# Optimization experiments

Measured on AMD Instinct MI355X. Metric: run time of the kernel, lower is better.

The kernel has to match this reference:

```python
import jax, jax.numpy as jnp
import numpy as np

H = 512; W = 512; WL = 8; SS = 4; DIM = 128; HEADS = 4; HD = DIM // HEADS; HID = 512
N = WL * WL                      # tokens per window = 64
NW = (H // WL) * (W // WL)       # num windows = 4096
EPS = 1e-5


def _rel_pos_index():
    # standard Swin relative position index for a WLxWL window
    coords = np.stack(np.meshgrid(np.arange(WL), np.arange(WL), indexing='ij')).reshape(2, -1)  # [2, N]
    rel = (coords[:, :, None] - coords[:, None, :]).transpose(1, 2, 0)  # [N, N, 2]
    rel[..., 0] += WL - 1
    rel[..., 1] += WL - 1
    rel[..., 0] *= 2 * WL - 1
    return jnp.asarray(rel.sum(-1))  # [N, N] in [0, (2WL-1)^2)


def _shift_attn_mask():
    # region ids 0/1/2 along each axis per the h_slices/w_slices loop, cnt = 3*h_id + w_id
    ids = np.zeros(H)
    ids[H - WL:H - SS] = 1
    ids[H - SS:] = 2
    img = 3.0 * ids[:, None] + ids[None, :]                     # [H, W]
    wnd = img.reshape(H // WL, WL, W // WL, WL).transpose(0, 2, 1, 3).reshape(NW, N)
    diff = wnd[:, None, :] - wnd[:, :, None]                    # [NW, N, N]
    return jnp.asarray(np.where(diff != 0, -100.0, 0.0).astype(np.float32))


REL_IDX = _rel_pos_index()
ATTN_MASK = _shift_attn_mask()


def _layernorm(v, w, b):
    mu = v.mean(-1, keepdims=True)
    var = v.var(-1, keepdims=True)
    return (v - mu) * jax.lax.rsqrt(var + EPS) * w + b


def setup_inputs() -> dict:
    key = jax.random.key(0)
    ks = jax.random.split(key, 10)
    s = 0.02
    return {
        'x': jax.random.normal(ks[0], (H * W, DIM), dtype=jnp.float32),
        'ln1_w': jnp.ones((DIM,), jnp.float32), 'ln1_b': jnp.zeros((DIM,), jnp.float32),
        'qkv_w': jax.random.normal(ks[1], (3 * DIM, DIM), jnp.float32) * s,
        'qkv_b': jnp.zeros((3 * DIM,), jnp.float32),
        'rel_bias': jax.random.normal(ks[2], ((2 * WL - 1) ** 2, HEADS), jnp.float32) * s,
        'proj_w': jax.random.normal(ks[3], (DIM, DIM), jnp.float32) * s,
        'proj_b': jnp.zeros((DIM,), jnp.float32),
        'ln2_w': jnp.ones((DIM,), jnp.float32), 'ln2_b': jnp.zeros((DIM,), jnp.float32),
        'mlp_w1': jax.random.normal(ks[4], (HID, DIM), jnp.float32) * s,
        'mlp_b1': jnp.zeros((HID,), jnp.float32),
        'mlp_w2': jax.random.normal(ks[5], (DIM, HID), jnp.float32) * s,
        'mlp_b2': jnp.zeros((DIM,), jnp.float32),
    }


def reference(x, ln1_w, ln1_b, qkv_w, qkv_b, rel_bias, proj_w, proj_b,
              ln2_w, ln2_b, mlp_w1, mlp_b1, mlp_w2, mlp_b2):
    skip = x
    xn = _layernorm(x, ln1_w, ln1_b).reshape(H, W, DIM)
    # cyclic shift
    xs = jnp.roll(xn, shift=(-SS, -SS), axis=(0, 1))
    # window partition -> [NW, N, DIM]
    xw = xs.reshape(H // WL, WL, W // WL, WL, DIM).transpose(0, 2, 1, 3, 4).reshape(NW, N, DIM)
    # qkv projection, split heads
    qkv = (xw @ qkv_w.T + qkv_b).reshape(NW, N, 3, HEADS, HD)
    q, k, v = qkv[:, :, 0], qkv[:, :, 1], qkv[:, :, 2]   # each [NW, N, HEADS, HD]
    scale = HD ** -0.5
    scores = jnp.einsum('wnhd,wmhd->whnm', q, k) * scale   # [NW, HEADS, N, N]
    bias = rel_bias[REL_IDX].transpose(2, 0, 1)            # [HEADS, N, N]
    scores = scores + bias[None] + ATTN_MASK[:, None]
    attn = jax.nn.softmax(scores, axis=-1)
    out = jnp.einsum('whnm,wmhd->wnhd', attn, v).reshape(NW, N, DIM)
    out = out @ proj_w.T + proj_b
    # window reverse
    xr = out.reshape(H // WL, W // WL, WL, WL, DIM).transpose(0, 2, 1, 3, 4).reshape(H, W, DIM)
    # reverse cyclic shift
    xr = jnp.roll(xr, shift=(SS, SS), axis=(0, 1)).reshape(H * W, DIM)
    x1 = skip + xr
    # FFN block
    h = _layernorm(x1, ln2_w, ln2_b)
    h = jax.nn.gelu(h @ mlp_w1.T + mlp_b1) @ mlp_w2.T + mlp_b2
    return x1 + h
```

## Files before the change

### kernel.cpp

```cpp
#include <hip/hip_runtime.h>
#include <hip/hip_bf16.h>


typedef __bf16 bf16x8 __attribute__((ext_vector_type(8)));
typedef __bf16 bf16x2 __attribute__((ext_vector_type(2)));
typedef float f32x4 __attribute__((ext_vector_type(4)));

#define MFMA16(a, b, c) __builtin_amdgcn_mfma_f32_16x16x32_bf16(a, b, c, 0, 0, 0)
#define LGKM_BARRIER() do { \
    asm volatile("s_waitcnt lgkmcnt(0)" ::: "memory"); \
    __builtin_amdgcn_s_barrier(); } while (0)

#define SS 4
#define XS 136
#define QKS 40
#define PSS 72
#define X1S 140

#define QKV_W_OFF 0
#define PROJ_W_OFF 98304
#define W1_OFF 131072
#define W2_OFF 262144
#define BIAS_OFF 393216

__device__ __forceinline__ int regid(int u) { return (u >= 508) ? 2 : ((u >= 504) ? 1 : 0); }

__global__ __launch_bounds__(256) void prep_kernel(
    const float* __restrict__ qkv_w, const float* __restrict__ proj_w,
    const float* __restrict__ w1, const float* __restrict__ w2,
    const float* __restrict__ rel_bias, unsigned char* __restrict__ ws) {
  int tid = blockIdx.x * 256 + threadIdx.x;
  __bf16* qw = (__bf16*)(ws + QKV_W_OFF);
  __bf16* pw = (__bf16*)(ws + PROJ_W_OFF);
  __bf16* w1b = (__bf16*)(ws + W1_OFF);
  __bf16* w2b = (__bf16*)(ws + W2_OFF);
  float* btbl = (float*)(ws + BIAS_OFF);
  if (tid < 49152) {
    int e = tid & 7, lane = (tid >> 3) & 63, kk = (tid >> 9) & 3;
    int f = tid >> 11;
    int h = f / 6, nt = f % 6;
    int j = (nt >> 1) * 128 + h * 32 + (nt & 1) * 16 + (lane & 15);
    int k = kk * 32 + (lane >> 4) * 8 + e;
    qw[tid] = (__bf16)qkv_w[j * 128 + k];
  }
  if (tid < 16384) {
    int e = tid & 7, lane = (tid >> 3) & 63, kk = (tid >> 9) & 3;
    int nt2 = (tid >> 11) & 1, wid = (tid >> 12) & 3;
    int j = wid * 32 + nt2 * 16 + (lane & 15);
    int k = kk * 32 + (lane >> 4) * 8 + e;
    pw[tid] = (__bf16)proj_w[j * 128 + k];
  }
  if (tid < 65536) {
    {
      int e = tid & 7, lane = (tid >> 3) & 63, kk = (tid >> 9) & 3;
      int nt = (tid >> 11) & 1, wid = (tid >> 12) & 7, c = (tid >> 15) & 1;
      int j = c * 256 + wid * 32 + nt * 16 + (lane & 15);
      int k = kk * 32 + (lane >> 4) * 8 + e;
      w1b[tid] = (__bf16)w1[j * 128 + k]; }
    { int e = tid & 7, lane = (tid >> 3) & 63, kk = (tid >> 9) & 15, wid = (tid >> 13) & 7;
      int j = wid * 16 + (lane & 15);
      int k = kk * 32 + (lane >> 4) * 8 + e;
      w2b[tid] = (__bf16)w2[j * 512 + k]; }
  }
  if (tid < 16384) {
    int i = tid & 3, lane = (tid >> 2) & 63;
    int kt = (tid >> 8) & 3, qt = (tid >> 10) & 3, h = (tid >> 12) & 3;
    int n = qt * 16 + (lane & 15);
    int m = kt * 16 + (lane >> 4) * 4 + i;
    int idx = ((n >> 3) - (m >> 3) + 7) * 15 + ((n & 7) - (m & 7) + 7);
    btbl[tid] = rel_bias[idx * 4 + h];
  }
}

__global__ __launch_bounds__(256, 2) void attn_kernel(
    const float* __restrict__ x, const float* __restrict__ ln1_w, const float* __restrict__ ln1_b,
    const float* __restrict__ qkv_b, const float* __restrict__ proj_b,
    const unsigned char* __restrict__ ws, float* __restrict__ out) {
  __shared__ __attribute__((aligned(16))) __bf16 xn[64 * XS];
  __shared__ __attribute__((aligned(16))) __bf16 wreg[4][5120];
  __shared__ __attribute__((aligned(16))) __bf16 vt[4][32 * PSS];
  __shared__ __attribute__((aligned(16))) int rid[64];

  const int w = blockIdx.x;
  const int wi = w >> 6, wj = w & 63;
  const int tid = threadIdx.x;
  const int wid = tid >> 6, lane = tid & 63;
  const int lr = lane & 15, lk = lane >> 4;
  const bool edge = (wi == 63) || (wj == 63);
  const f32x4 zero4 = {0.f, 0.f, 0.f, 0.f};

  const __bf16* qw = (const __bf16*)(ws + QKV_W_OFF);
  bf16x8 bw[6][4];
  float qb[6];
#pragma unroll
  for (int nt = 0; nt < 6; nt++) {
    qb[nt] = qkv_b[(nt >> 1) * 128 + wid * 32 + (nt & 1) * 16 + lr];
#pragma unroll
    for (int kk = 0; kk < 4; kk++)
      bw[nt][kk] = *(const bf16x8*)(qw + ((wid * 6 + nt) * 4 + kk) * 512 + lane * 8);
  }

  {
    int n = tid >> 2, q = tid & 3;
    int r = n >> 3, c = n & 7;
    int io = (wi * 8 + r + SS) & 511;
    int jo = (wj * 8 + c + SS) & 511;
    size_t gid = (size_t)io * 512 + jo;
    const float4* xp = (const float4*)(x + gid * 128 + q * 32);
    float4 xv[8];
    float s = 0.f, s2 = 0.f;
#pragma unroll
    for (int t = 0; t < 8; t++) {
      float4 v = xp[t]; xv[t] = v;
      s += v.x + v.y + v.z + v.w;
      s2 += v.x * v.x + v.y * v.y + v.z * v.z + v.w * v.w;
    }
    s += __shfl_xor(s, 1); s += __shfl_xor(s, 2);
    s2 += __shfl_xor(s2, 1); s2 += __shfl_xor(s2, 2);
    float mean = s * (1.f / 128.f);
    float var = s2 * (1.f / 128.f) - mean * mean;
    float rstd = rsqrtf(var + 1e-5f);
    const float4* wv = (const float4*)(ln1_w + q * 32);
    const float4* bv = (const float4*)(ln1_b + q * 32);
    __bf16* dst = xn + n * XS + q * 32;
#pragma unroll
    for (int t = 0; t < 8; t++) {
      float4 wt = wv[t], bt = bv[t], v = xv[t];
      dst[t * 4 + 0] = (__bf16)((v.x - mean) * rstd * wt.x + bt.x);
      dst[t * 4 + 1] = (__bf16)((v.y - mean) * rstd * wt.y + bt.y);
      dst[t * 4 + 2] = (__bf16)((v.z - mean) * rstd * wt.z + bt.z);
      dst[t * 4 + 3] = (__bf16)((v.w - mean) * rstd * wt.w + bt.w);
    }
    if (q == 0) rid[n] = 3 * regid(wi * 8 + r) + regid(wj * 8 + c);
  }
  LGKM_BARRIER();

  {
    const float scale = 0.17677669529663687f;
    __bf16* qbase = &wreg[wid][0];
    __bf16* kbase = &wreg[wid][2560];
    __bf16* vbase = &vt[wid][0];
#pragma unroll
    for (int st = 0; st < 4; st++) {
      bf16x8 a[4];
#pragma unroll
      for (int kk = 0; kk < 4; kk++)
        a[kk] = *(const bf16x8*)(xn + (st * 16 + lr) * XS + kk * 32 + lk * 8);
#pragma unroll
      for (int nt = 0; nt < 6; nt++) {
        f32x4 acc = zero4;
#pragma unroll
        for (int kk = 0; kk < 4; kk++) acc = MFMA16(a[kk], bw[nt][kk], acc);
        float bias = qb[nt];
        int dl = (nt & 1) * 16 + lr;
        if (nt < 2) {
#pragma unroll
          for (int i = 0; i < 4; i++)
            qbase[(st * 16 + lk * 4 + i) * QKS + dl] = (__bf16)((acc[i] + bias) * scale);
        } else if (nt < 4) {
#pragma unroll
          for (int i = 0; i < 4; i++)
            kbase[(st * 16 + lk * 4 + i) * QKS + dl] = (__bf16)(acc[i] + bias);
        } else {
#pragma unroll
          for (int i = 0; i < 4; i++)
            vbase[dl * PSS + st * 16 + lk * 4 + i] = (__bf16)(acc[i] + bias);
        }
      }
    }
  }

  const __bf16* pw = (const __bf16*)(ws + PROJ_W_OFF);
  bf16x8 pwf[2][4];
  float pb2[2];
#pragma unroll
  for (int nt2 = 0; nt2 < 2; nt2++) {
    pb2[nt2] = proj_b[wid * 32 + nt2 * 16 + lr];
#pragma unroll
    for (int kk = 0; kk < 4; kk++)
      pwf[nt2][kk] = *(const bf16x8*)(pw + ((wid * 2 + nt2) * 4 + kk) * 512 + lane * 8);
  }
  const float* btbl = (const float*)(ws + BIAS_OFF);
  f32x4 bc[4][4];
#pragma unroll
  for (int qt = 0; qt < 4; qt++)
#pragma unroll
    for (int kt = 0; kt < 4; kt++)
      bc[qt][kt] = *(const f32x4*)(btbl + ((wid * 4 + qt) * 4 + kt) * 256 + lane * 4);

  int gidx[4][4];
#pragma unroll
  for (int st = 0; st < 4; st++)
#pragma unroll
    for (int i = 0; i < 4; i++) {
      int rr = st * 16 + lk * 4 + i;
      int io = (wi * 8 + (rr >> 3) + SS) & 511;
      int jo = (wj * 8 + (rr & 7) + SS) & 511;
      gidx[st][i] = io * 512 + jo;
    }
  float xres[4][2][4];
#pragma unroll
  for (int st = 0; st < 4; st++)
#pragma unroll
    for (int nt2 = 0; nt2 < 2; nt2++)
#pragma unroll
      for (int i = 0; i < 4; i++)
        xres[st][nt2][i] = x[(size_t)gidx[st][i] * 128 + wid * 32 + nt2 * 16 + lr];

  {
    __bf16* reg0 = &wreg[wid][0];
    bf16x8 kf[4], qf[4], vf[2][2];
#pragma unroll
    for (int kt = 0; kt < 4; kt++)
      kf[kt] = *(const bf16x8*)(reg0 + 2560 + (kt * 16 + lr) * QKS + lk * 8);
#pragma unroll
    for (int qt = 0; qt < 4; qt++)
      qf[qt] = *(const bf16x8*)(reg0 + (qt * 16 + lr) * QKS + lk * 8);
#pragma unroll
    for (int dt = 0; dt < 2; dt++)
#pragma unroll
      for (int kk = 0; kk < 2; kk++)
        vf[dt][kk] = *(const bf16x8*)(&vt[wid][(dt * 16 + lr) * PSS + kk * 32 + lk * 8]);
    asm volatile("s_waitcnt lgkmcnt(0)" ::: "memory");
    __builtin_amdgcn_sched_barrier(0);

    int4 rk[4];
    if (edge) {
#pragma unroll
      for (int kt = 0; kt < 4; kt++) rk[kt] = *(const int4*)&rid[kt * 16 + lk * 4];
    }

#pragma unroll
    for (int qt = 0; qt < 4; qt++) {
      f32x4 s[4];
#pragma unroll
      for (int kt = 0; kt < 4; kt++) s[kt] = MFMA16(kf[kt], qf[qt], bc[qt][kt]);
      if (edge) {
        int rq = rid[qt * 16 + lr];
#pragma unroll
        for (int kt = 0; kt < 4; kt++) {
          s[kt][0] += (rk[kt].x != rq) ? -100.f : 0.f;
          s[kt][1] += (rk[kt].y != rq) ? -100.f : 0.f;
          s[kt][2] += (rk[kt].z != rq) ? -100.f : 0.f;
          s[kt][3] += (rk[kt].w != rq) ? -100.f : 0.f;
        }
      }
      float ex[4][4];
      float sum = 0.f;
#pragma unroll
      for (int kt = 0; kt < 4; kt++) {
#pragma unroll
        for (int i = 0; i < 4; i++) { ex[kt][i] = __expf(s[kt][i]); sum += ex[kt][i]; }
      }
      sum += __shfl_xor(sum, 16);
      sum += __shfl_xor(sum, 32);
      float inv = __builtin_amdgcn_rcpf(sum);
      __bf16* psrow = reg0 + (qt * 16 + lr) * PSS;
#pragma unroll
      for (int kt = 0; kt < 4; kt++) {
        bf16x2 p01 = {(__bf16)(ex[kt][0] * inv), (__bf16)(ex[kt][1] * inv)};
        bf16x2 p23 = {(__bf16)(ex[kt][2] * inv), (__bf16)(ex[kt][3] * inv)};
        *(bf16x2*)(psrow + kt * 16 + lk * 4) = p01;
        *(bf16x2*)(psrow + kt * 16 + lk * 4 + 2) = p23;
      }
#pragma unroll
      for (int dt = 0; dt < 2; dt++) {
        bf16x8 pa0 = *(const bf16x8*)(reg0 + (qt * 16 + lr) * PSS + lk * 8);
        bf16x8 pa1 = *(const bf16x8*)(reg0 + (qt * 16 + lr) * PSS + 32 + lk * 8);
        f32x4 acc = MFMA16(pa0, vf[dt][0], zero4);
        acc = MFMA16(pa1, vf[dt][1], acc);
#pragma unroll
        for (int i = 0; i < 4; i++)
          reg0[qt * 1152 + (lk * 4 + i) * QKS + dt * 16 + lr] = (__bf16)acc[i];
      }
    }
  }
  LGKM_BARRIER();

  {
#pragma unroll
    for (int st = 0; st < 4; st++) {
      bf16x8 ao[4];
#pragma unroll
      for (int kk = 0; kk < 4; kk++)
        ao[kk] = *(const bf16x8*)(&wreg[kk][st * 1152 + lr * QKS + lk * 8]);
#pragma unroll
      for (int nt2 = 0; nt2 < 2; nt2++) {
        f32x4 acc = zero4;
#pragma unroll
        for (int kk = 0; kk < 4; kk++) acc = MFMA16(ao[kk], pwf[nt2][kk], acc);
        int j = wid * 32 + nt2 * 16 + lr;
#pragma unroll
        for (int i = 0; i < 4; i++) {
          size_t off = (size_t)gidx[st][i] * 128 + j;
          out[off] = xres[st][nt2][i] + acc[i] + pb2[nt2];
        }
      }
    }
  }
}

__device__ __forceinline__ float gelu_sig(float x) {
  float e = exp2f(x * -2.4554826f);
  return x * __builtin_amdgcn_rcpf(1.f + e);
}

__global__ __launch_bounds__(512, 4) void mlp_kernel(
    const float* __restrict__ ln2_w, const float* __restrict__ ln2_b,
    const float* __restrict__ mlp_b1, const float* __restrict__ mlp_b2,
    const unsigned char* __restrict__ ws, float* __restrict__ out) {
  __shared__ __attribute__((aligned(16))) __bf16 xn[64 * 128];
  __shared__ __attribute__((aligned(16))) __bf16 hb[64 * 256];
  __shared__ __attribute__((aligned(16))) __bf16 x1b[64 * X1S];
  const int tid = threadIdx.x;
  const int wid = tid >> 6, lane = tid & 63;
  const int lr = lane & 15, lk = lane >> 4;
  const f32x4 zero4 = {0.f, 0.f, 0.f, 0.f};
  const int row0 = blockIdx.x * 64;

  const __bf16* w1r = (const __bf16*)(ws + W1_OFF);
  const __bf16* w2r = (const __bf16*)(ws + W2_OFF);

  float b1v[2][2];
#pragma unroll
  for (int c = 0; c < 2; c++)
#pragma unroll
    for (int nt = 0; nt < 2; nt++)
      b1v[c][nt] = mlp_b1[c * 256 + wid * 32 + nt * 16 + lr];
  float b2v = mlp_b2[wid * 16 + lr];

  {
    int n = tid >> 3, q = tid & 7;
    const float4* xp = (const float4*)(out + (size_t)(row0 + n) * 128 + q * 16);
    float4 xv[4];
    float s = 0.f, s2 = 0.f;
#pragma unroll
    for (int t = 0; t < 4; t++) {
      float4 v = xp[t]; xv[t] = v;
      s += v.x + v.y + v.z + v.w;
      s2 += v.x * v.x + v.y * v.y + v.z * v.z + v.w * v.w;
    }
    s += __shfl_xor(s, 1); s += __shfl_xor(s, 2); s += __shfl_xor(s, 4);
    s2 += __shfl_xor(s2, 1); s2 += __shfl_xor(s2, 2); s2 += __shfl_xor(s2, 4);
    float mean = s * (1.f / 128.f);
    float var = s2 * (1.f / 128.f) - mean * mean;
    float rstd = rsqrtf(var + 1e-5f);
    const float4* wv = (const float4*)(ln2_w + q * 16);
    const float4* bv = (const float4*)(ln2_b + q * 16);
    bf16x8 o[2], r[2];
#pragma unroll
    for (int t = 0; t < 4; t++) {
      float4 wt = wv[t], bt = bv[t], v = xv[t];
      o[t >> 1][(t & 1) * 4 + 0] = (__bf16)((v.x - mean) * rstd * wt.x + bt.x);
      o[t >> 1][(t & 1) * 4 + 1] = (__bf16)((v.y - mean) * rstd * wt.y + bt.y);
      o[t >> 1][(t & 1) * 4 + 2] = (__bf16)((v.z - mean) * rstd * wt.z + bt.z);
      o[t >> 1][(t & 1) * 4 + 3] = (__bf16)((v.w - mean) * rstd * wt.w + bt.w);
      r[t >> 1][(t & 1) * 4 + 0] = (__bf16)v.x;
      r[t >> 1][(t & 1) * 4 + 1] = (__bf16)v.y;
      r[t >> 1][(t & 1) * 4 + 2] = (__bf16)v.z;
      r[t >> 1][(t & 1) * 4 + 3] = (__bf16)v.w;
    }
    *(bf16x8*)(xn + n * 128 + (((q * 2 + 0) ^ (n & 15)) << 3)) = o[0];
    *(bf16x8*)(xn + n * 128 + (((q * 2 + 1) ^ (n & 15)) << 3)) = o[1];
    *(bf16x8*)(x1b + n * X1S + q * 16) = r[0];
    *(bf16x8*)(x1b + n * X1S + q * 16 + 8) = r[1];
  }
  __syncthreads();

  f32x4 macc[4] = {zero4, zero4, zero4, zero4};

#pragma unroll 1
  for (int c = 0; c < 2; c++) {
    {
      bf16x8 w1f[2][4];
#pragma unroll
      for (int nt = 0; nt < 2; nt++)
#pragma unroll
        for (int kk = 0; kk < 4; kk++)
          w1f[nt][kk] = *(const bf16x8*)(w1r + (((c * 8 + wid) * 2 + nt) * 4 + kk) * 512 + lane * 8);
#pragma unroll
      for (int st = 0; st < 4; st++) {
        bf16x8 a1[4];
#pragma unroll
        for (int kk = 0; kk < 4; kk++)
          a1[kk] = *(const bf16x8*)(xn + (st * 16 + lr) * 128 + (((kk * 4 + lk) ^ lr) << 3));
#pragma unroll
        for (int nt = 0; nt < 2; nt++) {
          f32x4 acc = zero4;
#pragma unroll
          for (int kk = 0; kk < 4; kk++) acc = MFMA16(a1[kk], w1f[nt][kk], acc);
          int slot = wid * 4 + nt * 2 + (lr >> 3);
#pragma unroll
          for (int i = 0; i < 4; i++) {
            int row = st * 16 + lk * 4 + i;
            hb[row * 256 + ((slot ^ (row & 15)) << 3) + (lr & 7)] =
                (__bf16)gelu_sig(acc[i] + b1v[c][nt]);
          }
        }
      }
    }
    __syncthreads();

    {
      bf16x8 w2f[8];
#pragma unroll
      for (int kks = 0; kks < 8; kks++)
        w2f[kks] = *(const bf16x8*)(w2r + (wid * 16 + c * 8 + kks) * 512 + lane * 8);
#pragma unroll
      for (int st = 0; st < 4; st++) {
#pragma unroll
        for (int kks = 0; kks < 8; kks++) {
          bf16x8 ah = *(const bf16x8*)(hb + (st * 16 + lr) * 256 + (((kks * 4 + lk) ^ lr) << 3));
          macc[st] = MFMA16(ah, w2f[kks], macc[st]);
        }
      }
    }
    __syncthreads();
  }

  {
    float* stg = (float*)hb;
#pragma unroll
    for (int st = 0; st < 4; st++)
#pragma unroll
      for (int i = 0; i < 4; i++) {
        int row = st * 16 + lk * 4 + i;
        int col = wid * 16 + lr;
        int sp = (col >> 2) ^ (((row >> 2) & 7) << 2);
        float x1v = (float)x1b[row * X1S + col];
        stg[row * 128 + sp * 4 + (col & 3)] = x1v + macc[st][i] + b2v;
      }
    __syncthreads();
    int half = lane >> 5, sl = lane & 31;
#pragma unroll
    for (int it = 0; it < 4; it++) {
      int row = wid * 8 + it * 2 + half;
      int sp = sl ^ (((row >> 2) & 7) << 2);
      f32x4 v = *(const f32x4*)(stg + row * 128 + sp * 4);
      *(f32x4*)(out + (size_t)(row0 + row) * 128 + sl * 4) = v;
    }
  }
}

extern "C" void kernel_launch(void* const* d_in, const int* in_sizes, int n_in,
                              void* d_out, int out_size, void* d_ws, size_t ws_size,
                              hipStream_t stream) {
  const float* x      = (const float*)d_in[0];
  const float* ln1_w  = (const float*)d_in[1];
  const float* ln1_b  = (const float*)d_in[2];
  const float* qkv_w  = (const float*)d_in[3];
  const float* qkv_b  = (const float*)d_in[4];
  const float* rel_b  = (const float*)d_in[5];
  const float* proj_w = (const float*)d_in[6];
  const float* proj_b = (const float*)d_in[7];
  const float* ln2_w  = (const float*)d_in[8];
  const float* ln2_b  = (const float*)d_in[9];
  const float* mlp_w1 = (const float*)d_in[10];
  const float* mlp_b1 = (const float*)d_in[11];
  const float* mlp_w2 = (const float*)d_in[12];
  const float* mlp_b2 = (const float*)d_in[13];
  float* out = (float*)d_out;
  unsigned char* ws = (unsigned char*)d_ws;

  prep_kernel<<<256, 256, 0, stream>>>(qkv_w, proj_w, mlp_w1, mlp_w2, rel_b, ws);
  attn_kernel<<<4096, 256, 0, stream>>>(x, ln1_w, ln1_b, qkv_b, proj_b, ws, out);
  mlp_kernel<<<4096, 512, 0, stream>>>(ln2_w, ln2_b, mlp_b1, mlp_b2, ws, out);
}
```

Baseline: 256.3 us.

## Split MLP hidden dimension into four chunks to shrink LDS and raise occupancy

The MLP kernel now processes the 512-wide hidden layer in four 128-wide chunks instead of two 256-wide ones, halving the hidden staging buffer in shared memory. It also reorders the W1 weight layout to match, folds the biases into the accumulator initial values, packs the shared buffers into one array, and raises the launch-bounds occupancy hint from 4 to 6. The aim is more resident workgroups per CU to hide memory latency, at the cost of twice as many barrier-separated phases per block.

New measurement: 238.8 us. 1.07x faster.

```diff
diff --git a/kernel.cpp b/kernel.cpp
--- a/kernel.cpp
+++ b/kernel.cpp
@@ -15,7 +15,7 @@
 #define XS 136
 #define QKS 40
 #define PSS 72
-#define X1S 140
+#define X1S 136
 
 #define QKV_W_OFF 0
 #define PROJ_W_OFF 98304
@@ -53,11 +53,12 @@
   if (tid < 65536) {
     {
       int e = tid & 7, lane = (tid >> 3) & 63, kk = (tid >> 9) & 3;
-      int nt = (tid >> 11) & 1, wid = (tid >> 12) & 7, c = (tid >> 15) & 1;
-      int j = c * 256 + wid * 32 + nt * 16 + (lane & 15);
+      int g = (tid >> 11) & 31;
+      int j = g * 16 + (lane & 15);
       int k = kk * 32 + (lane >> 4) * 8 + e;
       w1b[tid] = (__bf16)w1[j * 128 + k]; }
-    { int e = tid & 7, lane = (tid >> 3) & 63, kk = (tid >> 9) & 15, wid = (tid >> 13) & 7;
+    {
+      int e = tid & 7, lane = (tid >> 3) & 63, kk = (tid >> 9) & 15, wid = (tid >> 13) & 7;
       int j = wid * 16 + (lane & 15);
       int k = kk * 32 + (lane >> 4) * 8 + e;
       w2b[tid] = (__bf16)w2[j * 512 + k]; }
@@ -305,29 +306,27 @@
   return x * __builtin_amdgcn_rcpf(1.f + e);
 }
 
-__global__ __launch_bounds__(512, 4) void mlp_kernel(
+__global__ __launch_bounds__(512, 6) void mlp_kernel(
     const float* __restrict__ ln2_w, const float* __restrict__ ln2_b,
     const float* __restrict__ mlp_b1, const float* __restrict__ mlp_b2,
     const unsigned char* __restrict__ ws, float* __restrict__ out) {
-  __shared__ __attribute__((aligned(16))) __bf16 xn[64 * 128];
-  __shared__ __attribute__((aligned(16))) __bf16 hb[64 * 256];
-  __shared__ __attribute__((aligned(16))) __bf16 x1b[64 * X1S];
+  __shared__ __attribute__((aligned(16))) unsigned char smem[50176];
+  __bf16* xn  = (__bf16*)smem;
+  __bf16* hb  = (__bf16*)(smem + 16384);
+  __bf16* x1b = (__bf16*)(smem + 32768);
   const int tid = threadIdx.x;
   const int wid = tid >> 6, lane = tid & 63;
   const int lr = lane & 15, lk = lane >> 4;
-  const f32x4 zero4 = {0.f, 0.f, 0.f, 0.f};
   const int row0 = blockIdx.x * 64;
+  const int col = wid * 16 + lr;
 
   const __bf16* w1r = (const __bf16*)(ws + W1_OFF);
   const __bf16* w2r = (const __bf16*)(ws + W2_OFF);
 
-  float b1v[2][2];
-#pragma unroll
-  for (int c = 0; c < 2; c++)
-#pragma unroll
-    for (int nt = 0; nt < 2; nt++)
-      b1v[c][nt] = mlp_b1[c * 256 + wid * 32 + nt * 16 + lr];
-  float b2v = mlp_b2[wid * 16 + lr];
+  float b1v[4];
+#pragma unroll
+  for (int c = 0; c < 4; c++) b1v[c] = mlp_b1[c * 128 + wid * 16 + lr];
+  float b2v = mlp_b2[col];
 
   {
     int n = tid >> 3, q = tid & 7;
@@ -367,50 +366,48 @@
   }
   __syncthreads();
 
-  f32x4 macc[4] = {zero4, zero4, zero4, zero4};
+  f32x4 macc[4];
+#pragma unroll
+  for (int st = 0; st < 4; st++) macc[st] = (f32x4){b2v, b2v, b2v, b2v};
 
 #pragma unroll 1
-  for (int c = 0; c < 2; c++) {
+  for (int c = 0; c < 4; c++) {
     {
-      bf16x8 w1f[2][4];
-#pragma unroll
-      for (int nt = 0; nt < 2; nt++)
-#pragma unroll
-        for (int kk = 0; kk < 4; kk++)
-          w1f[nt][kk] = *(const bf16x8*)(w1r + (((c * 8 + wid) * 2 + nt) * 4 + kk) * 512 + lane * 8);
+      bf16x8 w1f[4];
+#pragma unroll
+      for (int kk = 0; kk < 4; kk++)
+        w1f[kk] = *(const bf16x8*)(w1r + ((c * 8 + wid) * 4 + kk) * 512 + lane * 8);
+      f32x4 bini = {b1v[c], b1v[c], b1v[c], b1v[c]};
+      int slot = wid * 2 + (lr >> 3);
 #pragma unroll
       for (int st = 0; st < 4; st++) {
         bf16x8 a1[4];
 #pragma unroll
         for (int kk = 0; kk < 4; kk++)
           a1[kk] = *(const bf16x8*)(xn + (st * 16 + lr) * 128 + (((kk * 4 + lk) ^ lr) << 3));
-#pragma unroll
-        for (int nt = 0; nt < 2; nt++) {
-          f32x4 acc = zero4;
-#pragma unroll
-          for (int kk = 0; kk < 4; kk++) acc = MFMA16(a1[kk], w1f[nt][kk], acc);
-          int slot = wid * 4 + nt * 2 + (lr >> 3);
-#pragma unroll
-          for (int i = 0; i < 4; i++) {
-            int row = st * 16 + lk * 4 + i;
-            hb[row * 256 + ((slot ^ (row & 15)) << 3) + (lr & 7)] =
-                (__bf16)gelu_sig(acc[i] + b1v[c][nt]);
-          }
+        f32x4 acc = bini;
+#pragma unroll
+        for (int kk = 0; kk < 4; kk++) acc = MFMA16(a1[kk], w1f[kk], acc);
+#pragma unroll
+        for (int i = 0; i < 4; i++) {
+          int row = st * 16 + lk * 4 + i;
+          hb[row * 128 + ((slot ^ (row & 15)) << 3) + (lr & 7)] =
+              (__bf16)gelu_sig(acc[i]);
         }
       }
     }
     __syncthreads();
 
     {
-      bf16x8 w2f[8];
-#pragma unroll
-      for (int kks = 0; kks < 8; kks++)
-        w2f[kks] = *(const bf16x8*)(w2r + (wid * 16 + c * 8 + kks) * 512 + lane * 8);
+      bf16x8 w2f[4];
+#pragma unroll
+      for (int kks = 0; kks < 4; kks++)
+        w2f[kks] = *(const bf16x8*)(w2r + (wid * 16 + c * 4 + kks) * 512 + lane * 8);
 #pragma unroll
       for (int st = 0; st < 4; st++) {
 #pragma unroll
-        for (int kks = 0; kks < 8; kks++) {
-          bf16x8 ah = *(const bf16x8*)(hb + (st * 16 + lr) * 256 + (((kks * 4 + lk) ^ lr) << 3));
+        for (int kks = 0; kks < 4; kks++) {
+          bf16x8 ah = *(const bf16x8*)(hb + (st * 16 + lr) * 128 + (((kks * 4 + lk) ^ lr) << 3));
           macc[st] = MFMA16(ah, w2f[kks], macc[st]);
         }
       }
@@ -419,16 +416,15 @@
   }
 
   {
-    float* stg = (float*)hb;
+    float* stg = (float*)smem;
 #pragma unroll
     for (int st = 0; st < 4; st++)
 #pragma unroll
       for (int i = 0; i < 4; i++) {
         int row = st * 16 + lk * 4 + i;
-        int col = wid * 16 + lr;
+        float x1v = (float)x1b[row * X1S + col];
         int sp = (col >> 2) ^ (((row >> 2) & 7) << 2);
-        float x1v = (float)x1b[row * X1S + col];
-        stg[row * 128 + sp * 4 + (col & 3)] = x1v + macc[st][i] + b2v;
+        stg[row * 128 + sp * 4 + (col & 3)] = x1v + macc[st][i];
       }
     __syncthreads();
     int half = lane >> 5, sl = lane & 31;
```
